# Optimization experiments

Hardware: AMD Instinct MI355X
Metric: run time of the kernel (lower is better)

The kernel has to match this reference:

```python
import jax, jax.numpy as jnp
import numpy as np

D = 256; HEADS = 8; DH = 32; LVLS = 3; PTS = 4; FF = 1024; FCD = 12544
SHAPES = ((100, 152), (50, 76), (25, 38))  # stride 8/16/32 maps for an 800x1216 image
INCH = (512, 1024, 2048)
N = 2; P_IMG = 1000


def sine_pos(h, w):
    # PositionEmbeddingSine, normalize=True, fully-valid mask
    eps = 1e-6; scale = 2.0 * np.pi
    y = jnp.cumsum(jnp.ones((h, w), jnp.float32), 0)
    x = jnp.cumsum(jnp.ones((h, w), jnp.float32), 1)
    y = y / (y[-1:, :] + eps) * scale
    x = x / (x[:, -1:] + eps) * scale
    dim_t = 10000.0 ** ((2.0 * (jnp.arange(128) // 2)).astype(jnp.float32) / 128.0)
    def inter(p):  # interleave sin/cos like torch.stack(...).flatten(3)
        return jnp.stack([jnp.sin(p[..., 0::2]), jnp.cos(p[..., 1::2])], -1).reshape(h, w, 128)
    return jnp.concatenate([inter(y[..., None] / dim_t), inter(x[..., None] / dim_t)], -1).reshape(h * w, D)


def bilinear(img, gx, gy):
    # F.grid_sample bilinear, align_corners=False, padding_mode='zeros'
    # img [C,H,W]; gx,gy in [-1,1] of any shape -> out [C, *gx.shape]
    C, H, W = img.shape
    x = ((gx + 1.0) * W - 1.0) * 0.5
    y = ((gy + 1.0) * H - 1.0) * 0.5
    x0 = jnp.floor(x); y0 = jnp.floor(y)
    wx = x - x0; wy = y - y0
    x0i = x0.astype(jnp.int32); y0i = y0.astype(jnp.int32)
    def g(xi, yi):
        ok = ((xi >= 0) & (xi < W) & (yi >= 0) & (yi < H)).astype(img.dtype)
        v = img[:, jnp.clip(yi, 0, H - 1), jnp.clip(xi, 0, W - 1)]
        return v * ok[None]
    return (g(x0i, y0i) * ((1 - wx) * (1 - wy))[None]
            + g(x0i + 1, y0i) * (wx * (1 - wy))[None]
            + g(x0i, y0i + 1) * ((1 - wx) * wy)[None]
            + g(x0i + 1, y0i + 1) * (wx * wy)[None])


def layernorm(x, g, b):
    mu = x.mean(-1, keepdims=True)
    var = ((x - mu) ** 2).mean(-1, keepdims=True)
    return (x - mu) / jnp.sqrt(var + 1e-5) * g + b


def _forward(feat0, feat1, feat2, point_coords, projw, projb, gng, gnb, level_embed,
             w_off, b_off, w_attn, b_attn, w_val, b_val, w_out, b_out,
             ln1_g, ln1_b, ln2_g, ln2_b, w_ff1, b_ff1, w_ff2, b_ff2, fc_w, fc_b):
    feats = (feat0, feat1, feat2)
    srcs = []; poss = []
    for l in range(LVLS):
        # input_proj: 1x1 conv + GroupNorm(32, 256)
        s = jnp.einsum('nchw,oc->nohw', feats[l], projw[l]) + projb[l][None, :, None, None]
        n, c, h, w = s.shape
        sg = s.reshape(n, 32, c // 32, h, w)
        mu = sg.mean((2, 3, 4), keepdims=True)
        var = ((sg - mu) ** 2).mean((2, 3, 4), keepdims=True)
        s = ((sg - mu) / jnp.sqrt(var + 1e-5)).reshape(n, c, h, w) * gng[l][None, :, None, None] + gnb[l][None, :, None, None]
        srcs.append(s.reshape(n, c, h * w).transpose(0, 2, 1))
        poss.append(sine_pos(h, w)[None] + level_embed[l][None, None, :])
    src = jnp.concatenate(srcs, 1)            # [N, Len, D]
    pos = jnp.concatenate(poss, 1)            # [1, Len, D] broadcast
    # reference points (valid_ratios == 1)
    refs = []
    for (h, w) in SHAPES:
        gy, gx = jnp.meshgrid((jnp.arange(h) + 0.5) / h, (jnp.arange(w) + 0.5) / w, indexing='ij')
        refs.append(jnp.stack([gx.ravel(), gy.ravel()], -1))
    ref = jnp.concatenate(refs, 0)            # [Len, 2] (x, y)
    Lq = src.shape[1]
    q = src + pos
    value = (src @ w_val.T + b_val).reshape(N, Lq, HEADS, DH)
    off = (q @ w_off.T + b_off).reshape(N, Lq, HEADS, LVLS, PTS, 2)
    aw = jax.nn.softmax((q @ w_attn.T + b_attn).reshape(N, Lq, HEADS, LVLS * PTS), -1).reshape(N, Lq, HEADS, LVLS, PTS)
    norm = jnp.array([[w, h] for (h, w) in SHAPES], jnp.float32)  # [L, 2] offset normalizer (W_, H_)
    locs = ref[None, :, None, None, None, :] + off / norm[None, None, None, :, None, :]  # [N,Lq,H,L,P,2]
    # MSDeformAttn core: per-level bilinear gather, accumulate weighted samples
    acc = jnp.zeros((N * HEADS, DH, Lq), src.dtype)
    start = 0
    for lvl, (h, w) in enumerate(SHAPES):
        v = value[:, start:start + h * w].transpose(0, 2, 3, 1).reshape(N * HEADS, DH, h, w)
        g = (2.0 * locs[:, :, :, lvl] - 1.0).transpose(0, 2, 1, 3, 4).reshape(N * HEADS, Lq, PTS, 2)
        s = jax.vmap(bilinear)(v, g[..., 0], g[..., 1])                 # [NH, DH, Lq, PTS]
        a = aw[:, :, :, lvl].transpose(0, 2, 1, 3).reshape(N * HEADS, 1, Lq, PTS)
        acc = acc + (s * a).sum(-1)
        start += h * w
    attn_out = acc.reshape(N, HEADS * DH, Lq).transpose(0, 2, 1) @ w_out.T + b_out
    x = layernorm(src + attn_out, ln1_g, ln1_b)
    ff = jax.nn.relu(x @ w_ff1.T + b_ff1) @ w_ff2.T + b_ff2
    x = layernorm(x + ff, ln2_g, ln2_b)
    # take level-0 tokens back to a feature map
    H0, W0 = SHAPES[0]
    mem = x.transpose(0, 2, 1)[:, :, :H0 * W0].reshape(N, D, H0, W0)
    # point_sample: grid_sample at 2*coords-1
    gpc = 2.0 * point_coords - 1.0
    pf = jax.vmap(bilinear)(mem, gpc[..., 0], gpc[..., 1])              # [N, D, P]
    pf = pf.transpose(0, 2, 1).reshape(N * P_IMG, D)
    # fc: Conv1d(256 -> 12544, k=1) + relu, then squeeze/permute
    return jax.nn.relu(pf @ fc_w.T + fc_b[None])


def setup_inputs() -> dict:
    key = jax.random.key(0)
    ki = iter(jax.random.split(key, 48))
    def rn(shape, scale):
        return jax.random.normal(next(ki), shape, jnp.float32) * scale
    d = {}
    d['feat0'] = jax.random.normal(next(ki), (N, 512, 100, 152), jnp.float32)
    d['feat1'] = jax.random.normal(next(ki), (N, 1024, 50, 76), jnp.float32)
    d['feat2'] = jax.random.normal(next(ki), (N, 2048, 25, 38), jnp.float32)
    d['point_coords'] = jax.random.uniform(next(ki), (N, P_IMG, 2), jnp.float32)
    d['gt_classes'] = jax.random.randint(next(ki), (N * P_IMG,), 0, 81)
    for l in range(LVLS):
        cin = INCH[l]
        d[f'proj{l}_w'] = rn((D, cin), 1.0 / np.sqrt(cin))
        d[f'proj{l}_b'] = jnp.zeros((D,), jnp.float32)
        d[f'gn{l}_g'] = jnp.ones((D,), jnp.float32)
        d[f'gn{l}_b'] = jnp.zeros((D,), jnp.float32)
    d['level_embed'] = rn((LVLS, D), 1.0)
    d['w_off'] = rn((HEADS * LVLS * PTS * 2, D), 0.01)
    d['b_off'] = rn((HEADS * LVLS * PTS * 2,), 0.2)
    d['w_attn'] = rn((HEADS * LVLS * PTS, D), 0.01)
    d['b_attn'] = jnp.zeros((HEADS * LVLS * PTS,), jnp.float32)
    d['w_val'] = rn((D, D), 1.0 / 16)
    d['b_val'] = jnp.zeros((D,), jnp.float32)
    d['w_out'] = rn((D, D), 1.0 / 16)
    d['b_out'] = jnp.zeros((D,), jnp.float32)
    d['ln1_g'] = jnp.ones((D,), jnp.float32); d['ln1_b'] = jnp.zeros((D,), jnp.float32)
    d['ln2_g'] = jnp.ones((D,), jnp.float32); d['ln2_b'] = jnp.zeros((D,), jnp.float32)
    d['w_ff1'] = rn((FF, D), 1.0 / 16); d['b_ff1'] = jnp.zeros((FF,), jnp.float32)
    d['w_ff2'] = rn((D, FF), 1.0 / 32); d['b_ff2'] = jnp.zeros((D,), jnp.float32)
    d['fc_w'] = rn((FCD, D), 1.0 / 16); d['fc_b'] = jnp.zeros((FCD,), jnp.float32)
    return d


def reference(feat0, feat1, feat2, point_coords, gt_classes,
              proj0_w, proj0_b, gn0_g, gn0_b, proj1_w, proj1_b, gn1_g, gn1_b,
              proj2_w, proj2_b, gn2_g, gn2_b, level_embed,
              w_off, b_off, w_attn, b_attn, w_val, b_val, w_out, b_out,
              ln1_g, ln1_b, ln2_g, ln2_b, w_ff1, b_ff1, w_ff2, b_ff2, fc_w, fc_b):
    out = _forward(feat0, feat1, feat2, point_coords,
                   (proj0_w, proj1_w, proj2_w), (proj0_b, proj1_b, proj2_b),
                   (gn0_g, gn1_g, gn2_g), (gn0_b, gn1_b, gn2_b), level_embed,
                   w_off, b_off, w_attn, b_attn, w_val, b_val, w_out, b_out,
                   ln1_g, ln1_b, ln2_g, ln2_b, w_ff1, b_ff1, w_ff2, b_ff2, fc_w, fc_b)
    return (out, gt_classes)
```

## Files before the change

### kernel.cpp

```cpp
#include <hip/hip_runtime.h>
#include <cstddef>
#include <cstdint>

#define D_MODEL 256
#define LQ 19950
#define NBATCH 2
#define NT (NBATCH*LQ)

typedef short  bf16x8 __attribute__((ext_vector_type(8)));
typedef float  f32x4  __attribute__((ext_vector_type(4)));
typedef unsigned short u16x8 __attribute__((ext_vector_type(8)));
typedef unsigned short u16x4 __attribute__((ext_vector_type(4)));

__device__ __forceinline__ unsigned short f2b(float f) {
  unsigned u = __float_as_uint(f);
  u += 0x7fff + ((u >> 16) & 1);
  return (unsigned short)(u >> 16);
}
__device__ __forceinline__ float b2f(unsigned short s) {
  return __uint_as_float(((unsigned)s) << 16);
}
__device__ __forceinline__ bf16x8 pack8(float4 a, float4 b) {
  bf16x8 r;
  r[0]=(short)f2b(a.x); r[1]=(short)f2b(a.y); r[2]=(short)f2b(a.z); r[3]=(short)f2b(a.w);
  r[4]=(short)f2b(b.x); r[5]=(short)f2b(b.y); r[6]=(short)f2b(b.z); r[7]=(short)f2b(b.w);
  return r;
}

__device__ __forceinline__ void tok_level(int tok, int& H, int& W, int& loff, int& lvl) {
  if (tok < 15200)      { lvl=0; H=100; W=152; loff=0; }
  else if (tok < 19000) { lvl=1; H=50;  W=76;  loff=15200; }
  else                  { lvl=2; H=25;  W=38;  loff=19000; }
}

#if __has_builtin(__builtin_amdgcn_global_load_lds)
#define HAVE_GLL 1
__device__ __forceinline__ void gload16(const void* g, void* lds_base_uniform) {
  __builtin_amdgcn_global_load_lds(
      (const __attribute__((address_space(1))) void*)g,
      (__attribute__((address_space(3))) void*)lds_base_uniform, 16, 0, 0);
}
#else
#define HAVE_GLL 0
#endif

template<bool ABF, int BMODE, bool CBF, bool RELU, bool ROWBIAS>
__global__ __launch_bounds__(256) void mgemm(
    const void* __restrict__ Av, const void* __restrict__ Bv,
    const float* __restrict__ bias, void* __restrict__ Cv,
    int M, int N, int K, int lda, int ldb, long sB, long sC, int zShift)
{
  __shared__ unsigned short As[64][72];
  __shared__ unsigned short Bs[64][72];
  const int tid = threadIdx.x;
  const int n0 = blockIdx.x * 64, m0 = blockIdx.y * 64;
  const int zb = blockIdx.z;
  const int n_b = zb >> zShift;
  const int kBase = (zb & ((1 << zShift) - 1)) * K;
  const int lane = tid & 63;
  const int wave = tid >> 6;
  const int l15 = lane & 15, q = lane >> 4;
  const int m_off = (wave >> 1) * 32, n_off = (wave & 1) * 32;
  f32x4 acc[2][2] = {};

  for (int k0 = kBase; k0 < kBase + K; k0 += 64) {
    {
      int row = tid >> 2, kc = (tid & 3) * 8;
      int gm = m0 + row;
      bf16x8 v0 = (bf16x8)0, v1 = (bf16x8)0;
      if (gm < M) {
        if constexpr (ABF) {
          const unsigned short* A = (const unsigned short*)Av;
          v0 = *(const bf16x8*)&A[(size_t)gm*lda + k0 + kc];
          v1 = *(const bf16x8*)&A[(size_t)gm*lda + k0 + kc + 32];
        } else {
          const float* A = (const float*)Av;
          const float* p = &A[(size_t)gm*lda + k0 + kc];
          v0 = pack8(*(const float4*)p,      *(const float4*)(p+4));
          v1 = pack8(*(const float4*)(p+32), *(const float4*)(p+36));
        }
      }
      *(bf16x8*)&As[row][kc]    = v0;
      *(bf16x8*)&As[row][kc+32] = v1;
    }
    if constexpr (BMODE == 1) {
      const float* Bp = (const float*)Bv + (size_t)n_b * sB;
      int kr = tid >> 3, nc = (tid & 7) * 8;
      #pragma unroll
      for (int half = 0; half < 2; ++half) {
        int kk = kr + half*32;
        const float* p = &Bp[(size_t)(k0+kk)*ldb + n0 + nc];
        float v[8];
        if (n0 + nc + 7 < N) {
          float2 a0 = *(const float2*)p,     a1 = *(const float2*)(p+2);
          float2 a2 = *(const float2*)(p+4), a3 = *(const float2*)(p+6);
          v[0]=a0.x; v[1]=a0.y; v[2]=a1.x; v[3]=a1.y;
          v[4]=a2.x; v[5]=a2.y; v[6]=a3.x; v[7]=a3.y;
        } else {
          #pragma unroll
          for (int i=0;i<8;++i) v[i] = (n0+nc+i < N) ? p[i] : 0.f;
        }
        #pragma unroll
        for (int i=0;i<8;++i) Bs[nc+i][kk] = f2b(v[i]);
      }
    }
    __syncthreads();
    #pragma unroll
    for (int s = 0; s < 2; ++s) {
      bf16x8 a0 = *(const bf16x8*)&As[m_off      + l15][s*32 + q*8];
      bf16x8 a1 = *(const bf16x8*)&As[m_off + 16 + l15][s*32 + q*8];
      bf16x8 b0 = *(const bf16x8*)&Bs[n_off      + l15][s*32 + q*8];
      bf16x8 b1 = *(const bf16x8*)&Bs[n_off + 16 + l15][s*32 + q*8];
      acc[0][0] = __builtin_amdgcn_mfma_f32_16x16x32_bf16(a0, b0, acc[0][0], 0,0,0);
      acc[0][1] = __builtin_amdgcn_mfma_f32_16x16x32_bf16(a0, b1, acc[0][1], 0,0,0);
      acc[1][0] = __builtin_amdgcn_mfma_f32_16x16x32_bf16(a1, b0, acc[1][0], 0,0,0);
      acc[1][1] = __builtin_amdgcn_mfma_f32_16x16x32_bf16(a1, b1, acc[1][1], 0,0,0);
    }
    __syncthreads();
  }
  float* Cf = (float*)Cv + (size_t)zb * sC;
  unsigned short* Cb = (unsigned short*)Cv + (size_t)zb * sC;
  #pragma unroll
  for (int r = 0; r < 2; ++r) {
    #pragma unroll
    for (int c = 0; c < 2; ++c) {
      #pragma unroll
      for (int v = 0; v < 4; ++v) {
        int gm = m0 + m_off + r*16 + q*4 + v;
        int gn = n0 + n_off + c*16 + l15;
        if (gm < M && gn < N) {
          float o = acc[r][c][v];
          if (bias) o += ROWBIAS ? bias[gm] : bias[gn];
          if (RELU) o = fmaxf(o, 0.f);
          if constexpr (CBF) Cb[(size_t)gm*N + gn] = f2b(o);
          else               Cf[(size_t)gm*N + gn] = o;
        }
      }
    }
  }
}

__global__ __launch_bounds__(256) void proj_reduce(
    const float* __restrict__ part, const float* __restrict__ bias,
    float* __restrict__ out, int HW, int S)
{
  int half = HW >> 1;
  int per_n = D_MODEL * half;
  int total = NBATCH * per_n;
  const float2* p2 = (const float2*)part;
  float2* o2 = (float2*)out;
  for (int i = blockIdx.x*256 + threadIdx.x; i < total; i += gridDim.x*256) {
    int n = i / per_n;
    int r = i - n*per_n;
    int o = r / half;
    int hw2 = r - o*half;
    float ax = 0.f, ay = 0.f;
    for (int s = 0; s < S; ++s) {
      float2 v = p2[((size_t)(n*S+s)*D_MODEL + o)*half + hw2];
      ax += v.x; ay += v.y;
    }
    float b = bias[o];
    o2[((size_t)n*D_MODEL + o)*half + hw2] = make_float2(ax+b, ay+b);
  }
}

template<bool CBF, bool RELU>
__global__ __launch_bounds__(512) void gemm_bb(
    const unsigned short* __restrict__ A, const unsigned short* __restrict__ B,
    const float* __restrict__ bias, void* __restrict__ Cv,
    int M, int N, int K, int lda, int ldb)
{
  __shared__ unsigned short SA[2][8192];
  __shared__ unsigned short SB[2][8192];
  const int tid = threadIdx.x;
  const int lane = tid & 63, wave = tid >> 6;
  const int nwg = gridDim.x * gridDim.y;
  const int flat = blockIdx.y * gridDim.x + blockIdx.x;
  const int qn = nwg >> 3, rr = nwg & 7;
  const int xcd = flat & 7, lid = flat >> 3;
  const int swz = (xcd < rr ? xcd*(qn+1) : rr*(qn+1) + (xcd-rr)*qn) + lid;
  const int n0 = (swz % gridDim.x) * 128;
  const int m0 = (swz / gridDim.x) * 128;

  const int l15 = lane & 15, q = lane >> 4;
  const int m_off = (wave >> 2) * 64, n_off = (wave & 3) * 32;
  const int sr = lane >> 3;
  const int ssl = (lane & 7) ^ sr;
  const int rs = l15 & 7;
  f32x4 acc[4][2] = {};

  const int nt = K >> 6;
  int cur = 0;

  #pragma unroll
  for (int c = 0; c < 2; ++c) {
    int ch = wave*2 + c;
    const unsigned short* ga = A + (size_t)(m0 + ch*8 + sr)*lda + ssl*8;
    const unsigned short* gb = B + (size_t)(n0 + ch*8 + sr)*ldb + ssl*8;
#if HAVE_GLL
    gload16(ga, &SA[0][ch*512]);
    gload16(gb, &SB[0][ch*512]);
#else
    *(bf16x8*)&SA[0][ch*512 + lane*8] = *(const bf16x8*)ga;
    *(bf16x8*)&SB[0][ch*512 + lane*8] = *(const bf16x8*)gb;
#endif
  }
  __syncthreads();

  for (int t = 0; t < nt; ++t) {
    if (t + 1 < nt) {
      int k1 = (t + 1) << 6;
      #pragma unroll
      for (int c = 0; c < 2; ++c) {
        int ch = wave*2 + c;
        const unsigned short* ga = A + (size_t)(m0 + ch*8 + sr)*lda + k1 + ssl*8;
        const unsigned short* gb = B + (size_t)(n0 + ch*8 + sr)*ldb + k1 + ssl*8;
#if HAVE_GLL
        gload16(ga, &SA[cur^1][ch*512]);
        gload16(gb, &SB[cur^1][ch*512]);
#else
        *(bf16x8*)&SA[cur^1][ch*512 + lane*8] = *(const bf16x8*)ga;
        *(bf16x8*)&SB[cur^1][ch*512 + lane*8] = *(const bf16x8*)gb;
#endif
      }
    }
    #pragma unroll
    for (int s = 0; s < 2; ++s) {
      int ps = ((s*4 + q) ^ rs) * 8;
      bf16x8 af[4], bfr[2];
      #pragma unroll
      for (int i = 0; i < 4; ++i)
        af[i] = *(const bf16x8*)&SA[cur][(m_off + i*16 + l15)*64 + ps];
      #pragma unroll
      for (int j = 0; j < 2; ++j)
        bfr[j] = *(const bf16x8*)&SB[cur][(n_off + j*16 + l15)*64 + ps];
      #pragma unroll
      for (int i = 0; i < 4; ++i)
        #pragma unroll
        for (int j = 0; j < 2; ++j)
          acc[i][j] = __builtin_amdgcn_mfma_f32_16x16x32_bf16(af[i], bfr[j], acc[i][j], 0,0,0);
    }
    __syncthreads();
    cur ^= 1;
  }

  float* Cf = (float*)Cv;
  unsigned short* Cb = (unsigned short*)Cv;
  #pragma unroll
  for (int i = 0; i < 4; ++i) {
    #pragma unroll
    for (int j = 0; j < 2; ++j) {
      #pragma unroll
      for (int v = 0; v < 4; ++v) {
        int gm = m0 + m_off + i*16 + q*4 + v;
        int gn = n0 + n_off + j*16 + l15;
        if (gm < M && gn < N) {
          float o = acc[i][j][v];
          if (bias) o += bias[gn];
          if (RELU) o = fmaxf(o, 0.f);
          if constexpr (CBF) Cb[(size_t)gm*N + gn] = f2b(o);
          else               Cf[(size_t)gm*N + gn] = o;
        }
      }
    }
  }
}

struct W7 { const float* src[7]; unsigned short* dst[7]; int nv[7]; };
__global__ __launch_bounds__(256) void wconv(W7 w)
{
  int s = blockIdx.y;
  const float4* src = (const float4*)w.src[s];
  unsigned short* dst = w.dst[s];
  int n = w.nv[s];
  for (int i = blockIdx.x*256 + threadIdx.x; i < n; i += gridDim.x*256) {
    float4 v = src[i];
    u16x4 o = { f2b(v.x), f2b(v.y), f2b(v.z), f2b(v.w) };
    *(u16x4*)(dst + (size_t)i*4) = o;
  }
}

__global__ __launch_bounds__(288) void biascat(
    const float* __restrict__ b_off, const float* __restrict__ b_attn,
    float* __restrict__ out)
{
  int i = threadIdx.x;
  out[i] = (i < 192) ? b_off[i] : b_attn[i - 192];
}

__global__ __launch_bounds__(256) void gn_partial(
    const float* __restrict__ s, float* __restrict__ partials, int HW)
{
  int g = blockIdx.x, n = blockIdx.y, c = blockIdx.z;
  const float4* base = (const float4*)(s + ((size_t)n*D_MODEL + g*8) * HW);
  int nvec = (8*HW) >> 2;
  float sum = 0.f, sq = 0.f;
  for (int j = c*256 + threadIdx.x; j < nvec; j += 2048) {
    float4 v = base[j];
    sum += v.x+v.y+v.z+v.w;
    sq  += v.x*v.x+v.y*v.y+v.z*v.z+v.w*v.w;
  }
  #pragma unroll
  for (int m=32;m;m>>=1){ sum += __shfl_xor(sum,m,64); sq += __shfl_xor(sq,m,64); }
  __shared__ float s1[4], s2[4];
  int w = threadIdx.x >> 6;
  if ((threadIdx.x & 63) == 0) { s1[w]=sum; s2[w]=sq; }
  __syncthreads();
  if (threadIdx.x == 0) {
    partials[(((size_t)n*32+g)*8 + c)*2]     = s1[0]+s1[1]+s1[2]+s1[3];
    partials[(((size_t)n*32+g)*8 + c)*2 + 1] = s2[0]+s2[1]+s2[2]+s2[3];
  }
}

__global__ __launch_bounds__(64) void gn_finalize(
    const float* __restrict__ partials, float* __restrict__ stats, int HW)
{
  int t = threadIdx.x;
  float S = 0.f, Q = 0.f;
  #pragma unroll
  for (int c = 0; c < 8; ++c) {
    S += partials[((size_t)t*8 + c)*2];
    Q += partials[((size_t)t*8 + c)*2 + 1];
  }
  float inv = 1.f/(float)(8*HW);
  float mu = S*inv;
  float var = Q*inv - mu*mu;
  stats[(size_t)t*2]   = mu;
  stats[(size_t)t*2+1] = rsqrtf(var + 1e-5f);
}

__global__ __launch_bounds__(256) void gn_apply(
    const float* __restrict__ s, const float* __restrict__ stats,
    const float* __restrict__ gw, const float* __restrict__ gb,
    float* __restrict__ src, int HW, int loff)
{
  __shared__ float T[32][33];
  int tx = threadIdx.x & 31, ty = threadIdx.x >> 5;
  int hw0 = blockIdx.x*32, o0 = blockIdx.y*32, n = blockIdx.z;
  const float* base = s + (size_t)n*D_MODEL*HW;
  #pragma unroll
  for (int it=0; it<4; ++it) {
    int ol = ty + it*8;
    int o = o0 + ol;
    int hw = hw0 + tx;
    float v = 0.f;
    if (hw < HW) {
      int grp = o >> 3;
      float mu   = stats[((size_t)n*32+grp)*2];
      float rstd = stats[((size_t)n*32+grp)*2+1];
      v = (base[(size_t)o*HW + hw] - mu)*rstd*gw[o] + gb[o];
    }
    T[ol][tx] = v;
  }
  __syncthreads();
  #pragma unroll
  for (int it=0; it<4; ++it) {
    int tl = ty + it*8;
    int tok = hw0 + tl;
    if (tok < HW) {
      src[((size_t)n*LQ + loff + tok)*D_MODEL + o0 + tx] = T[tx][tl];
    }
  }
}

__global__ __launch_bounds__(256) void compute_q(
    const float* __restrict__ src, const float* __restrict__ level_embed,
    unsigned short* __restrict__ q, unsigned short* __restrict__ srcbf)
{
  int row = blockIdx.x;
  int d = threadIdx.x;
  int tok = row % LQ;
  int H,W,loff,lvl; tok_level(tok,H,W,loff,lvl);
  int hw = tok - loff;
  int i = hw / W, j = hw % W;
  const float TWO_PI = 6.28318530717958647692f;
  float yv = (float)(i+1) / ((float)H + 1e-6f) * TWO_PI;
  float xv = (float)(j+1) / ((float)W + 1e-6f) * TWO_PI;
  int m = (d & 127) >> 1;
  float invt = __expf((float)m * -0.14391156516f);
  float ang = ((d < 128) ? yv : xv) * invt;
  float pe = (d & 1) ? __cosf(ang) : __sinf(ang);
  size_t idx = (size_t)row*D_MODEL + d;
  float sv = src[idx];
  q[idx] = f2b(sv + pe + level_embed[lvl*D_MODEL + d]);
  srcbf[idx] = f2b(sv);
}

__global__ __launch_bounds__(256) void deform_sample(
    const unsigned short* __restrict__ value, const unsigned short* __restrict__ offaw,
    unsigned short* __restrict__ accb)
{
  int idx = blockIdx.x*256 + threadIdx.x;
  if (idx >= NT*8*4) return;
  int quarter = idx & 3;
  int h = (idx >> 2) & 7;
  int row = idx >> 5;
  int tok = row % LQ;
  int n = row / LQ;
  int Ht,Wt,lofft,lvlt; tok_level(tok,Ht,Wt,lofft,lvlt);
  int hw = tok - lofft;
  int ti = hw / Wt, tj = hw % Wt;
  float gxr = ((float)tj + 0.5f) / (float)Wt;
  float gyr = ((float)ti + 0.5f) / (float)Ht;
  const unsigned short* offr = offaw + (size_t)row*288 + h*24;
  const unsigned short* awr  = offaw + (size_t)row*288 + 192 + h*12;
  float off[24];
  {
    u16x8 o0 = *(const u16x8*)offr;
    u16x8 o1 = *(const u16x8*)(offr+8);
    u16x8 o2 = *(const u16x8*)(offr+16);
    #pragma unroll
    for (int c=0;c<8;++c){ off[c]=b2f(o0[c]); off[8+c]=b2f(o1[c]); off[16+c]=b2f(o2[c]); }
  }
  float lg[12];
  {
    u16x4 a0 = *(const u16x4*)awr;
    u16x4 a1 = *(const u16x4*)(awr+4);
    u16x4 a2 = *(const u16x4*)(awr+8);
    #pragma unroll
    for (int c=0;c<4;++c){ lg[c]=b2f(a0[c]); lg[4+c]=b2f(a1[c]); lg[8+c]=b2f(a2[c]); }
  }
  float mx = -1e30f;
  #pragma unroll
  for (int i=0;i<12;++i) mx = fmaxf(mx, lg[i]);
  float ssum = 0.f;
  #pragma unroll
  for (int i=0;i<12;++i){ lg[i] = __expf(lg[i]-mx); ssum += lg[i]; }
  float sinv = 1.f/ssum;
  float acc[8] = {0.f,0.f,0.f,0.f,0.f,0.f,0.f,0.f};
  const int HH[3]={100,50,25}, WW[3]={152,76,38}, OO[3]={0,15200,19000};
  int chbase = h*32 + quarter*8;
  #pragma unroll
  for (int lvl=0; lvl<3; ++lvl) {
    const int H=HH[lvl], W=WW[lvl], lo=OO[lvl];
    #pragma unroll
    for (int p=0; p<4; ++p) {
      float ox = off[lvl*8 + p*2];
      float oy = off[lvl*8 + p*2 + 1];
      float a  = lg[lvl*4 + p] * sinv;
      float x = (gxr + ox / (float)W) * (float)W - 0.5f;
      float y = (gyr + oy / (float)H) * (float)H - 0.5f;
      float x0f = floorf(x), y0f = floorf(y);
      float wx = x - x0f, wy = y - y0f;
      int x0 = (int)x0f, y0 = (int)y0f;
      float tw[4] = { (1.f-wx)*(1.f-wy)*a, wx*(1.f-wy)*a, (1.f-wx)*wy*a, wx*wy*a };
      #pragma unroll
      for (int t=0; t<4; ++t) {
        int xi = x0 + (t & 1), yi = y0 + (t >> 1);
        if (xi >= 0 && xi < W && yi >= 0 && yi < H) {
          const float w = tw[t];
          const unsigned short* vr = value + ((size_t)(n*LQ + lo + yi*W + xi)*D_MODEL + chbase);
          u16x8 v = *(const u16x8*)vr;
          #pragma unroll
          for (int jj=0;jj<8;++jj) acc[jj] += w * b2f(v[jj]);
        }
      }
    }
  }
  unsigned short* o = accb + (size_t)row*D_MODEL + chbase;
  u16x8 ov;
  #pragma unroll
  for (int jj=0;jj<8;++jj) ov[jj] = f2b(acc[jj]);
  *(u16x8*)o = ov;
}

template<bool EMITBF>
__global__ __launch_bounds__(256) void ln_add(
    const float* __restrict__ A, const float* __restrict__ B,
    const float* __restrict__ g, const float* __restrict__ b,
    float* __restrict__ out, unsigned short* __restrict__ outbf, int rows)
{
  int wid = (blockIdx.x * 256 + threadIdx.x) >> 6;
  int lane = threadIdx.x & 63;
  if (wid >= rows) return;
  size_t base = (size_t)wid * D_MODEL;
  float4 va = *(const float4*)&A[base + lane*4];
  float4 vb = *(const float4*)&B[base + lane*4];
  float v[4] = {va.x+vb.x, va.y+vb.y, va.z+vb.z, va.w+vb.w};
  float s = v[0]+v[1]+v[2]+v[3];
  #pragma unroll
  for (int m=32; m; m>>=1) s += __shfl_xor(s, m, 64);
  float mu = s * (1.f/256.f);
  float qq = 0.f;
  #pragma unroll
  for (int i=0;i<4;++i){ float d=v[i]-mu; qq += d*d; }
  #pragma unroll
  for (int m=32; m; m>>=1) qq += __shfl_xor(qq, m, 64);
  float rstd = rsqrtf(qq*(1.f/256.f) + 1e-5f);
  float o[4];
  #pragma unroll
  for (int i=0;i<4;++i){
    int d = lane*4+i;
    o[i] = (v[i]-mu)*rstd*g[d] + b[d];
  }
  *(float4*)&out[base + lane*4] = make_float4(o[0],o[1],o[2],o[3]);
  if constexpr (EMITBF) {
    u16x4 ob = { f2b(o[0]), f2b(o[1]), f2b(o[2]), f2b(o[3]) };
    *(u16x4*)&outbf[base + lane*4] = ob;
  }
}

__global__ __launch_bounds__(256) void point_sample(
    const float* __restrict__ x2, const float* __restrict__ pc,
    unsigned short* __restrict__ pf)
{
  int pidx = blockIdx.x;
  int n = pidx / 1000;
  float px = pc[(size_t)pidx*2], py = pc[(size_t)pidx*2+1];
  float x = ((2.f*px)*152.f - 1.f)*0.5f;
  float y = ((2.f*py)*100.f - 1.f)*0.5f;
  float x0f=floorf(x), y0f=floorf(y);
  float wx=x-x0f, wy=y-y0f;
  int x0=(int)x0f, y0=(int)y0f;
  int d = threadIdx.x;
  float accv = 0.f;
  #pragma unroll
  for (int t=0;t<4;++t) {
    int xi = x0 + (t&1), yi = y0 + (t>>1);
    float w = ((t&1)?wx:(1.f-wx)) * ((t>>1)?wy:(1.f-wy));
    if (xi>=0 && xi<152 && yi>=0 && yi<100) {
      accv += w * x2[((size_t)(n*LQ + yi*152 + xi))*D_MODEL + d];
    }
  }
  pf[(size_t)pidx*D_MODEL + d] = f2b(accv);
}

__global__ void copy_gt(const int* __restrict__ gt, float* __restrict__ out, int nels)
{
  int i = blockIdx.x*256 + threadIdx.x;
  if (i < nels) out[i] = (float)gt[i];
}

extern "C" void kernel_launch(void* const* d_in, const int* in_sizes, int n_in,
                              void* d_out, int out_size, void* d_ws, size_t ws_size,
                              hipStream_t stream)
{
  const float* feat[3]  = {(const float*)d_in[0], (const float*)d_in[1], (const float*)d_in[2]};
  const float* pc       = (const float*)d_in[3];
  const int*   gt       = (const int*)d_in[4];
  const float* projw[3] = {(const float*)d_in[5],  (const float*)d_in[9],  (const float*)d_in[13]};
  const float* projb[3] = {(const float*)d_in[6],  (const float*)d_in[10], (const float*)d_in[14]};
  const float* gng[3]   = {(const float*)d_in[7],  (const float*)d_in[11], (const float*)d_in[15]};
  const float* gnb[3]   = {(const float*)d_in[8],  (const float*)d_in[12], (const float*)d_in[16]};
  const float* level_embed = (const float*)d_in[17];
  const float* w_off  = (const float*)d_in[18];
  const float* b_off  = (const float*)d_in[19];
  const float* w_attn = (const float*)d_in[20];
  const float* b_attn = (const float*)d_in[21];
  const float* w_val  = (const float*)d_in[22];
  const float* b_val  = (const float*)d_in[23];
  const float* w_out  = (const float*)d_in[24];
  const float* b_out  = (const float*)d_in[25];
  const float* ln1g   = (const float*)d_in[26];
  const float* ln1b   = (const float*)d_in[27];
  const float* ln2g   = (const float*)d_in[28];
  const float* ln2b   = (const float*)d_in[29];
  const float* wff1   = (const float*)d_in[30];
  const float* bff1   = (const float*)d_in[31];
  const float* wff2   = (const float*)d_in[32];
  const float* bff2   = (const float*)d_in[33];
  const float* fcw    = (const float*)d_in[34];
  const float* fcb    = (const float*)d_in[35];

  float* ws    = (float*)d_ws;
  float* s_tmp = ws;
  unsigned short* q_b     = (unsigned short*)(s_tmp + 10214400);
  unsigned short* value_b = q_b + 10214400;
  float* srcb  = (float*)(value_b + 10214400);
  float* xreg  = srcb + 10214400;
  unsigned short* offaw   = (unsigned short*)(xreg + 10214400);
  unsigned short* wbf     = offaw + 11491200;
  float* stats    = (float*)(wbf + 3940352);
  float* partials = stats + 128;
  float* boffaw   = partials + 1024;

  unsigned short* wv_bf  = wbf;
  unsigned short* wof_bf = wbf + 65536;
  unsigned short* wat_bf = wbf + 114688;
  unsigned short* wou_bf = wbf + 139264;
  unsigned short* wf1_bf = wbf + 204800;
  unsigned short* wf2_bf = wbf + 466944;
  unsigned short* wfc_bf = wbf + 729088;

  float* kpart = xreg;
  unsigned short* src_bf = (unsigned short*)xreg;
  unsigned short* acc_b = q_b;
  unsigned short* xb_bf = offaw;
  unsigned short* hbuf  = (unsigned short*)s_tmp;
  unsigned short* pf    = value_b;
  float* ybuf = srcb;
  float* x2   = s_tmp;

  W7 w7;
  w7.src[0]=w_val;  w7.dst[0]=wv_bf;  w7.nv[0]=65536/4;
  w7.src[1]=w_off;  w7.dst[1]=wof_bf; w7.nv[1]=49152/4;
  w7.src[2]=w_attn; w7.dst[2]=wat_bf; w7.nv[2]=24576/4;
  w7.src[3]=w_out;  w7.dst[3]=wou_bf; w7.nv[3]=65536/4;
  w7.src[4]=wff1;   w7.dst[4]=wf1_bf; w7.nv[4]=262144/4;
  w7.src[5]=wff2;   w7.dst[5]=wf2_bf; w7.nv[5]=262144/4;
  w7.src[6]=fcw;    w7.dst[6]=wfc_bf; w7.nv[6]=3211264/4;
  wconv<<<dim3(512, 7), 256, 0, stream>>>(w7);
  biascat<<<1, 288, 0, stream>>>(b_off, b_attn, boffaw);

  const int HWs[3]  = {15200, 3800, 950};
  const int Cins[3] = {512, 1024, 2048};
  const int LOFF[3] = {0, 15200, 19000};
  const int ZSH[3]  = {0, 1, 2};

  for (int l = 0; l < 3; ++l) {
    int HW = HWs[l], K = Cins[l];
    int S = 1 << ZSH[l];
    int KC = K / S;
    if (S == 1) {
      mgemm<false,1,false,false,true><<<dim3((HW+63)/64, 4, NBATCH), 256, 0, stream>>>(
          projw[l], feat[l], projb[l], s_tmp, D_MODEL, HW, KC, K, HW,
          (long)K*HW, (long)D_MODEL*HW, 0);
    } else {
      mgemm<false,1,false,false,true><<<dim3((HW+63)/64, 4, NBATCH*S), 256, 0, stream>>>(
          projw[l], feat[l], nullptr, kpart, D_MODEL, HW, KC, K, HW,
          (long)K*HW, (long)D_MODEL*HW, ZSH[l]);
      int total2 = NBATCH * D_MODEL * (HW >> 1);
      int gr = (total2 + 255) / 256; if (gr > 2048) gr = 2048;
      proj_reduce<<<gr, 256, 0, stream>>>(kpart, projb[l], s_tmp, HW, S);
    }
    gn_partial<<<dim3(32, NBATCH, 8), 256, 0, stream>>>(s_tmp, partials, HW);
    gn_finalize<<<1, 64, 0, stream>>>(partials, stats, HW);
    gn_apply<<<dim3((HW+31)/32, 8, NBATCH), 256, 0, stream>>>(
        s_tmp, stats, gng[l], gnb[l], srcb, HW, LOFF[l]);
  }

  compute_q<<<NT, 256, 0, stream>>>(srcb, level_embed, q_b, src_bf);

  int gm128 = (NT + 127) / 128;
  gemm_bb<true,false><<<dim3(2, gm128), 512, 0, stream>>>(
      src_bf, wv_bf, b_val, value_b, NT, 256, 256, 256, 256);
  gemm_bb<true,false><<<dim3(3, gm128), 512, 0, stream>>>(
      q_b, wof_bf, boffaw, offaw, NT, 288, 256, 256, 256);

  deform_sample<<<(NT*8*4 + 255)/256, 256, 0, stream>>>(value_b, offaw, acc_b);

  gemm_bb<false,false><<<dim3(2, gm128), 512, 0, stream>>>(
      acc_b, wou_bf, b_out, s_tmp, NT, 256, 256, 256, 256);
  ln_add<true><<<(NT+3)/4, 256, 0, stream>>>(srcb, s_tmp, ln1g, ln1b, xreg, xb_bf, NT);

  gemm_bb<true,true><<<dim3(8, gm128), 512, 0, stream>>>(
      xb_bf, wf1_bf, bff1, hbuf, NT, 1024, 256, 256, 256);
  gemm_bb<false,false><<<dim3(2, gm128), 512, 0, stream>>>(
      hbuf, wf2_bf, bff2, ybuf, NT, 256, 1024, 1024, 1024);

  ln_add<false><<<(NT+3)/4, 256, 0, stream>>>(xreg, ybuf, ln2g, ln2b, x2, nullptr, NT);

  point_sample<<<2000, 256, 0, stream>>>(x2, pc, pf);
  gemm_bb<false,true><<<dim3(12544/128, (2000+127)/128), 512, 0, stream>>>(
      pf, wfc_bf, fcb, (float*)d_out, 2000, 12544, 256, 256, 256);
  copy_gt<<<8, 256, 0, stream>>>(gt, (float*)d_out + (size_t)2000*12544, 2000);
}
```

Measured before the change: 537.7 us.

## Fuse value/offset GEMMs, fold GN finalize, fast-path interior bilinear sampling

Merges the value projection and offset/attention projection GEMMs into one launch that picks operands by column block, and folds the GroupNorm finalize step into gn_apply so each block computes its own group statistics. Deformable sampling precomputes per-level base coordinates and adds an interior fast path that loads all four bilinear corners without per-corner bounds checks. Token-level index math is simplified with constant divisors. These cut launch overhead and ALU/branch cost, at the price of some redundant stats computation per block and a specialized GEMM kernel.

```diff
diff --git a/kernel.cpp b/kernel.cpp
--- a/kernel.cpp
+++ b/kernel.cpp
@@ -25,12 +25,6 @@
   r[0]=(short)f2b(a.x); r[1]=(short)f2b(a.y); r[2]=(short)f2b(a.z); r[3]=(short)f2b(a.w);
   r[4]=(short)f2b(b.x); r[5]=(short)f2b(b.y); r[6]=(short)f2b(b.z); r[7]=(short)f2b(b.w);
   return r;
-}
-
-__device__ __forceinline__ void tok_level(int tok, int& H, int& W, int& loff, int& lvl) {
-  if (tok < 15200)      { lvl=0; H=100; W=152; loff=0; }
-  else if (tok < 19000) { lvl=1; H=50;  W=76;  loff=15200; }
-  else                  { lvl=2; H=25;  W=38;  loff=19000; }
 }
 
 #if __has_builtin(__builtin_amdgcn_global_load_lds)
@@ -266,6 +260,107 @@
   }
 }
 
+__global__ __launch_bounds__(512) void gemm_vo(
+    const unsigned short* __restrict__ Asrc, const unsigned short* __restrict__ Aq,
+    const unsigned short* __restrict__ Bv,   const unsigned short* __restrict__ Bo,
+    const float* __restrict__ bias_v, const float* __restrict__ bias_o,
+    unsigned short* __restrict__ Cv, unsigned short* __restrict__ Co, int M)
+{
+  __shared__ unsigned short SA[2][8192];
+  __shared__ unsigned short SB[2][8192];
+  const int tid = threadIdx.x;
+  const int lane = tid & 63, wave = tid >> 6;
+  const int nwg = gridDim.x * gridDim.y;
+  const int flat = blockIdx.y * gridDim.x + blockIdx.x;
+  const int qn = nwg >> 3, rr = nwg & 7;
+  const int xcd = flat & 7, lid = flat >> 3;
+  const int swz = (xcd < rr ? xcd*(qn+1) : rr*(qn+1) + (xcd-rr)*qn) + lid;
+  const int colid = swz % gridDim.x;
+  const int m0 = (swz / gridDim.x) * 128;
+
+  const unsigned short* A; const unsigned short* B;
+  const float* bias; unsigned short* C; int N, n0;
+  if (colid < 2) { A = Asrc; B = Bv; bias = bias_v; C = Cv; N = 256; n0 = colid*128; }
+  else           { A = Aq;   B = Bo; bias = bias_o; C = Co; N = 288; n0 = (colid-2)*128; }
+
+  const int l15 = lane & 15, q = lane >> 4;
+  const int m_off = (wave >> 2) * 64, n_off = (wave & 3) * 32;
+  const int sr = lane >> 3;
+  const int ssl = (lane & 7) ^ sr;
+  const int rs = l15 & 7;
+  f32x4 acc[4][2] = {};
+  const int nt = 4;
+  int cur = 0;
+
+  #pragma unroll
+  for (int c = 0; c < 2; ++c) {
+    int ch = wave*2 + c;
+    const unsigned short* ga = A + (size_t)(m0 + ch*8 + sr)*256 + ssl*8;
+    const unsigned short* gb = B + (size_t)(n0 + ch*8 + sr)*256 + ssl*8;
+#if HAVE_GLL
+    gload16(ga, &SA[0][ch*512]);
+    gload16(gb, &SB[0][ch*512]);
+#else
+    *(bf16x8*)&SA[0][ch*512 + lane*8] = *(const bf16x8*)ga;
+    *(bf16x8*)&SB[0][ch*512 + lane*8] = *(const bf16x8*)gb;
+#endif
+  }
+  __syncthreads();
+
+  for (int t = 0; t < nt; ++t) {
+    if (t + 1 < nt) {
+      int k1 = (t + 1) << 6;
+      #pragma unroll
+      for (int c = 0; c < 2; ++c) {
+        int ch = wave*2 + c;
+        const unsigned short* ga = A + (size_t)(m0 + ch*8 + sr)*256 + k1 + ssl*8;
+        const unsigned short* gb = B + (size_t)(n0 + ch*8 + sr)*256 + k1 + ssl*8;
+#if HAVE_GLL
+        gload16(ga, &SA[cur^1][ch*512]);
+        gload16(gb, &SB[cur^1][ch*512]);
+#else
+        *(bf16x8*)&SA[cur^1][ch*512 + lane*8] = *(const bf16x8*)ga;
+        *(bf16x8*)&SB[cur^1][ch*512 + lane*8] = *(const bf16x8*)gb;
+#endif
+      }
+    }
+    #pragma unroll
+    for (int s = 0; s < 2; ++s) {
+      int ps = ((s*4 + q) ^ rs) * 8;
+      bf16x8 af[4], bfr[2];
+      #pragma unroll
+      for (int i = 0; i < 4; ++i)
+        af[i] = *(const bf16x8*)&SA[cur][(m_off + i*16 + l15)*64 + ps];
+      #pragma unroll
+      for (int j = 0; j < 2; ++j)
+        bfr[j] = *(const bf16x8*)&SB[cur][(n_off + j*16 + l15)*64 + ps];
+      #pragma unroll
+      for (int i = 0; i < 4; ++i)
+        #pragma unroll
+        for (int j = 0; j < 2; ++j)
+          acc[i][j] = __builtin_amdgcn_mfma_f32_16x16x32_bf16(af[i], bfr[j], acc[i][j], 0,0,0);
+    }
+    __syncthreads();
+    cur ^= 1;
+  }
+
+  #pragma unroll
+  for (int i = 0; i < 4; ++i) {
+    #pragma unroll
+    for (int j = 0; j < 2; ++j) {
+      #pragma unroll
+      for (int v = 0; v < 4; ++v) {
+        int gm = m0 + m_off + i*16 + q*4 + v;
+        int gn = n0 + n_off + j*16 + l15;
+        if (gm < M && gn < N) {
+          float o = acc[i][j][v] + bias[gn];
+          C[(size_t)gm*N + gn] = f2b(o);
+        }
+      }
+    }
+  }
+}
+
 struct W7 { const float* src[7]; unsigned short* dst[7]; int nv[7]; };
 __global__ __launch_bounds__(256) void wconv(W7 w)
 {
@@ -312,31 +407,30 @@
   }
 }
 
-__global__ __launch_bounds__(64) void gn_finalize(
-    const float* __restrict__ partials, float* __restrict__ stats, int HW)
-{
-  int t = threadIdx.x;
-  float S = 0.f, Q = 0.f;
-  #pragma unroll
-  for (int c = 0; c < 8; ++c) {
-    S += partials[((size_t)t*8 + c)*2];
-    Q += partials[((size_t)t*8 + c)*2 + 1];
-  }
-  float inv = 1.f/(float)(8*HW);
-  float mu = S*inv;
-  float var = Q*inv - mu*mu;
-  stats[(size_t)t*2]   = mu;
-  stats[(size_t)t*2+1] = rsqrtf(var + 1e-5f);
-}
-
 __global__ __launch_bounds__(256) void gn_apply(
-    const float* __restrict__ s, const float* __restrict__ stats,
+    const float* __restrict__ s, const float* __restrict__ partials,
     const float* __restrict__ gw, const float* __restrict__ gb,
     float* __restrict__ src, int HW, int loff)
 {
   __shared__ float T[32][33];
+  __shared__ float smu[4], srs[4];
   int tx = threadIdx.x & 31, ty = threadIdx.x >> 5;
   int hw0 = blockIdx.x*32, o0 = blockIdx.y*32, n = blockIdx.z;
+  if (threadIdx.x < 4) {
+    int g = (o0 >> 3) + threadIdx.x;
+    float S = 0.f, Q = 0.f;
+    #pragma unroll
+    for (int c = 0; c < 8; ++c) {
+      S += partials[(((size_t)n*32+g)*8 + c)*2];
+      Q += partials[(((size_t)n*32+g)*8 + c)*2 + 1];
+    }
+    float inv = 1.f/(float)(8*HW);
+    float mu = S*inv;
+    float var = Q*inv - mu*mu;
+    smu[threadIdx.x] = mu;
+    srs[threadIdx.x] = rsqrtf(var + 1e-5f);
+  }
+  __syncthreads();
   const float* base = s + (size_t)n*D_MODEL*HW;
   #pragma unroll
   for (int it=0; it<4; ++it) {
@@ -345,10 +439,7 @@
     int hw = hw0 + tx;
     float v = 0.f;
     if (hw < HW) {
-      int grp = o >> 3;
-      float mu   = stats[((size_t)n*32+grp)*2];
-      float rstd = stats[((size_t)n*32+grp)*2+1];
-      v = (base[(size_t)o*HW + hw] - mu)*rstd*gw[o] + gb[o];
+      v = (base[(size_t)o*HW + hw] - smu[ol>>3])*srs[ol>>3]*gw[o] + gb[o];
     }
     T[ol][tx] = v;
   }
@@ -369,10 +460,11 @@
 {
   int row = blockIdx.x;
   int d = threadIdx.x;
-  int tok = row % LQ;
-  int H,W,loff,lvl; tok_level(tok,H,W,loff,lvl);
-  int hw = tok - loff;
-  int i = hw / W, j = hw % W;
+  int tok = (row >= LQ) ? row - LQ : row;
+  int H, W, lvl, i, j;
+  if (tok < 15200)      { lvl=0; H=100; W=152; int hw=tok;        i=hw/152; j=hw-i*152; }
+  else if (tok < 19000) { lvl=1; H=50;  W=76;  int hw=tok-15200;  i=hw/76;  j=hw-i*76;  }
+  else                  { lvl=2; H=25;  W=38;  int hw=tok-19000;  i=hw/38;  j=hw-i*38;  }
   const float TWO_PI = 6.28318530717958647692f;
   float yv = (float)(i+1) / ((float)H + 1e-6f) * TWO_PI;
   float xv = (float)(j+1) / ((float)W + 1e-6f) * TWO_PI;
@@ -395,13 +487,32 @@
   int quarter = idx & 3;
   int h = (idx >> 2) & 7;
   int row = idx >> 5;
-  int tok = row % LQ;
-  int n = row / LQ;
-  int Ht,Wt,lofft,lvlt; tok_level(tok,Ht,Wt,lofft,lvlt);
-  int hw = tok - lofft;
-  int ti = hw / Wt, tj = hw % Wt;
-  float gxr = ((float)tj + 0.5f) / (float)Wt;
-  float gyr = ((float)ti + 0.5f) / (float)Ht;
+  int n = (row >= LQ) ? 1 : 0;
+  int tok = row - n*LQ;
+
+  float bxs0, bxs1, bxs2, bys0, bys1, bys2;
+  if (tok < 15200) {
+    int ti = tok/152, tj = tok - ti*152;
+    float bx = tj + 0.5f, by = ti + 0.5f;
+    bxs0 = bx - 0.5f;         bys0 = by - 0.5f;
+    bxs1 = bx*0.5f - 0.5f;    bys1 = by*0.5f - 0.5f;
+    bxs2 = bx*0.25f - 0.5f;   bys2 = by*0.25f - 0.5f;
+  } else if (tok < 19000) {
+    int hw = tok - 15200; int ti = hw/76, tj = hw - ti*76;
+    float bx = tj + 0.5f, by = ti + 0.5f;
+    bxs0 = bx*2.f - 0.5f;     bys0 = by*2.f - 0.5f;
+    bxs1 = bx - 0.5f;         bys1 = by - 0.5f;
+    bxs2 = bx*0.5f - 0.5f;    bys2 = by*0.5f - 0.5f;
+  } else {
+    int hw = tok - 19000; int ti = hw/38, tj = hw - ti*38;
+    float bx = tj + 0.5f, by = ti + 0.5f;
+    bxs0 = bx*4.f - 0.5f;     bys0 = by*4.f - 0.5f;
+    bxs1 = bx*2.f - 0.5f;     bys1 = by*2.f - 0.5f;
+    bxs2 = bx - 0.5f;         bys2 = by - 0.5f;
+  }
+  const float bxs[3] = {bxs0, bxs1, bxs2};
+  const float bys[3] = {bys0, bys1, bys2};
+
   const unsigned short* offr = offaw + (size_t)row*288 + h*24;
   const unsigned short* awr  = offaw + (size_t)row*288 + 192 + h*12;
   float off[24];
@@ -427,32 +538,47 @@
   #pragma unroll
   for (int i=0;i<12;++i){ lg[i] = __expf(lg[i]-mx); ssum += lg[i]; }
   float sinv = 1.f/ssum;
+
   float acc[8] = {0.f,0.f,0.f,0.f,0.f,0.f,0.f,0.f};
   const int HH[3]={100,50,25}, WW[3]={152,76,38}, OO[3]={0,15200,19000};
   int chbase = h*32 + quarter*8;
   #pragma unroll
   for (int lvl=0; lvl<3; ++lvl) {
     const int H=HH[lvl], W=WW[lvl], lo=OO[lvl];
+    const unsigned short* vbase = value + ((size_t)(n*LQ + lo)*D_MODEL) + chbase;
     #pragma unroll
     for (int p=0; p<4; ++p) {
       float ox = off[lvl*8 + p*2];
       float oy = off[lvl*8 + p*2 + 1];
       float a  = lg[lvl*4 + p] * sinv;
-      float x = (gxr + ox / (float)W) * (float)W - 0.5f;
-      float y = (gyr + oy / (float)H) * (float)H - 0.5f;
+      float x = bxs[lvl] + ox;
+      float y = bys[lvl] + oy;
       float x0f = floorf(x), y0f = floorf(y);
       float wx = x - x0f, wy = y - y0f;
       int x0 = (int)x0f, y0 = (int)y0f;
-      float tw[4] = { (1.f-wx)*(1.f-wy)*a, wx*(1.f-wy)*a, (1.f-wx)*wy*a, wx*wy*a };
-      #pragma unroll
-      for (int t=0; t<4; ++t) {
-        int xi = x0 + (t & 1), yi = y0 + (t >> 1);
-        if (xi >= 0 && xi < W && yi >= 0 && yi < H) {
-          const float w = tw[t];
-          const unsigned short* vr = value + ((size_t)(n*LQ + lo + yi*W + xi)*D_MODEL + chbase);
-          u16x8 v = *(const u16x8*)vr;
-          #pragma unroll
-          for (int jj=0;jj<8;++jj) acc[jj] += w * b2f(v[jj]);
+      float w00 = (1.f-wx)*(1.f-wy)*a, w10 = wx*(1.f-wy)*a;
+      float w01 = (1.f-wx)*wy*a,       w11 = wx*wy*a;
+      if ((unsigned)x0 < (unsigned)(W-1) && (unsigned)y0 < (unsigned)(H-1)) {
+        const unsigned short* b00 = vbase + (size_t)(y0*W + x0)*D_MODEL;
+        u16x8 v00 = *(const u16x8*)b00;
+        u16x8 v10 = *(const u16x8*)(b00 + D_MODEL);
+        u16x8 v01 = *(const u16x8*)(b00 + W*D_MODEL);
+        u16x8 v11 = *(const u16x8*)(b00 + W*D_MODEL + D_MODEL);
+        #pragma unroll
+        for (int c=0;c<8;++c)
+          acc[c] += w00*b2f(v00[c]) + w10*b2f(v10[c]) + w01*b2f(v01[c]) + w11*b2f(v11[c]);
+      } else {
+        float tw[4] = { w00, w10, w01, w11 };
+        #pragma unroll
+        for (int t=0; t<4; ++t) {
+          int xi = x0 + (t & 1), yi = y0 + (t >> 1);
+          if (xi >= 0 && xi < W && yi >= 0 && yi < H) {
+            const float w = tw[t];
+            const unsigned short* vr = vbase + (size_t)(yi*W + xi)*D_MODEL;
+            u16x8 v = *(const u16x8*)vr;
+            #pragma unroll
+            for (int jj=0;jj<8;++jj) acc[jj] += w * b2f(v[jj]);
+          }
         }
       }
     }
@@ -570,8 +696,7 @@
   float* xreg  = srcb + 10214400;
   unsigned short* offaw   = (unsigned short*)(xreg + 10214400);
   unsigned short* wbf     = offaw + 11491200;
-  float* stats    = (float*)(wbf + 3940352);
-  float* partials = stats + 128;
+  float* partials = (float*)(wbf + 3940352);
   float* boffaw   = partials + 1024;
 
   unsigned short* wv_bf  = wbf;
@@ -624,18 +749,15 @@
       proj_reduce<<<gr, 256, 0, stream>>>(kpart, projb[l], s_tmp, HW, S);
     }
     gn_partial<<<dim3(32, NBATCH, 8), 256, 0, stream>>>(s_tmp, partials, HW);
-    gn_finalize<<<1, 64, 0, stream>>>(partials, stats, HW);
     gn_apply<<<dim3((HW+31)/32, 8, NBATCH), 256, 0, stream>>>(
-        s_tmp, stats, gng[l], gnb[l], srcb, HW, LOFF[l]);
+        s_tmp, partials, gng[l], gnb[l], srcb, HW, LOFF[l]);
   }
 
   compute_q<<<NT, 256, 0, stream>>>(srcb, level_embed, q_b, src_bf);
 
   int gm128 = (NT + 127) / 128;
-  gemm_bb<true,false><<<dim3(2, gm128), 512, 0, stream>>>(
-      src_bf, wv_bf, b_val, value_b, NT, 256, 256, 256, 256);
-  gemm_bb<true,false><<<dim3(3, gm128), 512, 0, stream>>>(
-      q_b, wof_bf, boffaw, offaw, NT, 288, 256, 256, 256);
+  gemm_vo<<<dim3(5, gm128), 512, 0, stream>>>(
+      src_bf, q_b, wv_bf, wof_bf, b_val, boffaw, value_b, offaw, NT);
 
   deform_sample<<<(NT*8*4 + 255)/256, 256, 0, stream>>>(value_b, offaw, acc_b);
 
```

Measured after the change: 508.6 us. 1.06x faster.
